# Kernel optimization log

Measured on AMD Instinct MI355X. Metric: run time of the kernel, lower is better.

Reference implementation:

```python
import jax, jax.numpy as jnp
import numpy as np

N, F_IN, HID, NH1, NCLS = 8192, 256, 64, 4, 16
LRELU_ALPHA = 0.2  # tf.nn.leaky_relu default


def setup_inputs() -> dict:
    key = jax.random.key(0)
    ks = jax.random.split(key, 12)
    s = 0.05
    seq = jax.random.normal(ks[0], (1, N, F_IN), jnp.float32)
    # sparse-ish adjacency -> additive mask bias (0 on edges, -1e9 elsewhere)
    adj = jax.random.uniform(ks[1], (N, N)) < 0.005
    adj = adj | jnp.eye(N, dtype=bool)
    bias_mat = jnp.where(adj, 0.0, -1e9).astype(jnp.float32)[None]  # [1,N,N]
    return {
        "seq": seq,
        "bias_mat": bias_mat,
        "W1": jax.random.normal(ks[2], (NH1, F_IN, HID), jnp.float32) * s,
        "a1_src": jax.random.normal(ks[3], (NH1, HID, 1), jnp.float32) * s,
        "a1_dst": jax.random.normal(ks[4], (NH1, HID, 1), jnp.float32) * s,
        "b1_src": jnp.zeros((NH1, 1), jnp.float32),
        "b1_dst": jnp.zeros((NH1, 1), jnp.float32),
        "bias1": jnp.zeros((NH1, HID), jnp.float32),
        "W2": jax.random.normal(ks[5], (1, NH1 * HID, NCLS), jnp.float32) * s,
        "a2_src": jax.random.normal(ks[6], (1, NCLS, 1), jnp.float32) * s,
        "a2_dst": jax.random.normal(ks[7], (1, NCLS, 1), jnp.float32) * s,
        "b2_src": jnp.zeros((1, 1), jnp.float32),
        "b2_dst": jnp.zeros((1, 1), jnp.float32),
        "bias2": jnp.zeros((1, NCLS), jnp.float32),
    }


def _gat_layer(x, bias_mat, W, a_src, a_dst, b_src, b_dst, bias_out):
    # x: [N, Fin]; W: [nh, Fin, H]; bias_mat: [1, N, N]
    fts = jnp.einsum('nf,hfd->hnd', x, W)                      # Conv1D(k=1, no bias)
    f1 = jnp.einsum('hnd,hdo->hno', fts, a_src) + b_src[:, None, :]  # [nh,N,1]
    f2 = jnp.einsum('hnd,hdo->hno', fts, a_dst) + b_dst[:, None, :]  # [nh,N,1]
    logits = f1 + jnp.swapaxes(f2, 1, 2)                       # [nh,N,N]
    coefs = jax.nn.softmax(jax.nn.leaky_relu(logits, LRELU_ALPHA) + bias_mat, axis=-1)
    vals = jnp.einsum('hnm,hmd->hnd', coefs, fts)              # [nh,N,H]
    return vals + bias_out[:, None, :]


def reference(seq, bias_mat, W1, a1_src, a1_dst, b1_src, b1_dst, bias1,
              W2, a2_src, a2_dst, b2_src, b2_dst, bias2):
    x = seq[0]  # [N, F_IN]; batch dim is 1
    # layer 1: NH1 heads, elu activation, concat over heads
    h = jax.nn.elu(_gat_layer(x, bias_mat, W1, a1_src, a1_dst, b1_src, b1_dst, bias1))
    h1 = jnp.transpose(h, (1, 0, 2)).reshape(N, NH1 * HID)     # tf.concat(heads, -1)
    # output layer: 1 head, identity activation, averaged over final heads (=1)
    out = _gat_layer(h1, bias_mat, W2, a2_src, a2_dst, b2_src, b2_dst, bias2)
    logits = out[0] / 1.0                                      # add_n/final_sum
    return logits[None]  # [1, N, NCLS]
```

## Files before the change

kernel.cpp:

```cpp
#include <hip/hip_runtime.h>
#include <hip/hip_bf16.h>
#include <math.h>

#define NN    8192
#define FIN   256
#define HID   64
#define NH    4
#define NC    16
#define MAXD  128
#define ALPHA 0.2f
#define KC    32

typedef float nfloat4 __attribute__((ext_vector_type(4)));
__device__ __forceinline__ float4 ldnt4(const float4* p) {
    nfloat4 v = __builtin_nontemporal_load((const nfloat4*)p);
    return make_float4(v.x, v.y, v.z, v.w);
}

__global__ __launch_bounds__(256) void k_gemm(
    const float* __restrict__ seq, const float* __restrict__ W1,
    const float* __restrict__ a1s, const float* __restrict__ a1d,
    const float* __restrict__ b1s, const float* __restrict__ b1d,
    float* __restrict__ fts1, float* __restrict__ f1v, float* __restrict__ f2v)
{
    __shared__ union {
        struct { float xsT[KC][68]; float w[KC][68]; } g;
        struct { float r1[64][17];  float r2[64][17]; } gr;
    } S;
    const int t = threadIdx.x, b = blockIdx.x;
    const int head = b & 3, rowbase = (b >> 2) * 64;
    const int tr = t >> 4, tc = t & 15;

    float acc[4][4] = {};
    for (int kc = 0; kc < FIN / KC; ++kc) {
        #pragma unroll
        for (int i = 0; i < 2; ++i) {
            const int lin = t + i*256;
            const int row = lin >> 3, kq = lin & 7;
            const float4 v = *(const float4*)(seq + (size_t)(rowbase + row)*FIN + kc*KC + kq*4);
            S.g.xsT[kq*4+0][row] = v.x;
            S.g.xsT[kq*4+1][row] = v.y;
            S.g.xsT[kq*4+2][row] = v.z;
            S.g.xsT[kq*4+3][row] = v.w;
        }
        #pragma unroll
        for (int i = 0; i < 2; ++i) {
            const int lin = t + i*256;
            const int k = lin >> 4, dq = lin & 15;
            *(float4*)&S.g.w[k][dq*4] =
                *(const float4*)(W1 + ((size_t)head*FIN + kc*KC + k)*HID + dq*4);
        }
        __syncthreads();
        #pragma unroll 8
        for (int k = 0; k < KC; ++k) {
            const float4 aa = *(const float4*)&S.g.xsT[k][tr*4];
            const float4 bb = *(const float4*)&S.g.w[k][tc*4];
            acc[0][0] += aa.x*bb.x; acc[0][1] += aa.x*bb.y; acc[0][2] += aa.x*bb.z; acc[0][3] += aa.x*bb.w;
            acc[1][0] += aa.y*bb.x; acc[1][1] += aa.y*bb.y; acc[1][2] += aa.y*bb.z; acc[1][3] += aa.y*bb.w;
            acc[2][0] += aa.z*bb.x; acc[2][1] += aa.z*bb.y; acc[2][2] += aa.z*bb.z; acc[2][3] += aa.z*bb.w;
            acc[3][0] += aa.w*bb.x; acc[3][1] += aa.w*bb.y; acc[3][2] += aa.w*bb.z; acc[3][3] += aa.w*bb.w;
        }
        __syncthreads();
    }
    float p1[4], p2[4];
    #pragma unroll
    for (int i = 0; i < 4; ++i) {
        const int node = rowbase + tr*4 + i;
        float4 o; o.x = acc[i][0]; o.y = acc[i][1]; o.z = acc[i][2]; o.w = acc[i][3];
        *(float4*)&fts1[((size_t)node*NH + head)*HID + tc*4] = o;
        float s1 = 0.f, s2 = 0.f;
        #pragma unroll
        for (int j = 0; j < 4; ++j) {
            s1 += acc[i][j] * a1s[head*HID + tc*4 + j];
            s2 += acc[i][j] * a1d[head*HID + tc*4 + j];
        }
        p1[i] = s1; p2[i] = s2;
    }
    #pragma unroll
    for (int i = 0; i < 4; ++i) {
        S.gr.r1[tr*4 + i][tc] = p1[i];
        S.gr.r2[tr*4 + i][tc] = p2[i];
    }
    __syncthreads();
    if (t < 64) {
        float s1 = b1s[head], s2 = b1d[head];
        #pragma unroll
        for (int q = 0; q < 16; ++q) { s1 += S.gr.r1[t][q]; s2 += S.gr.r2[t][q]; }
        f1v[(rowbase + t)*NH + head] = s1;
        f2v[(rowbase + t)*NH + head] = s2;
    }
}

__global__ __launch_bounds__(256) void k_scan_attn(
    const float* __restrict__ bias, const float* __restrict__ fts1,
    const float* __restrict__ f1v4, const float* __restrict__ f2v4,
    const float* __restrict__ bias1, const float* __restrict__ W2,
    const float* __restrict__ a2s, const float* __restrict__ a2d,
    const float* __restrict__ b2s, const float* __restrict__ b2d,
    int* __restrict__ deg, int* __restrict__ cols,
    float* __restrict__ fts2, float* __restrict__ g1, float* __restrict__ g2)
{
    __shared__ int    colsS[4][MAXD];
    __shared__ float4 coefS[4][MAXD];
    __shared__ float  h1S[4][NH*HID];

    const int t = threadIdx.x, w = t >> 6, lane = t & 63;
    const int row = blockIdx.x*4 + w;
    const unsigned long long lt = (1ull << lane) - 1ull;

    colsS[w][lane] = 0; colsS[w][64 + lane] = 0;

    const float4* rp = (const float4*)(bias + (size_t)row * NN);
    float4 vv[8];
    #pragma unroll
    for (int k = 0; k < 8; ++k) vv[k] = ldnt4(rp + k*64 + lane);
    int base = 0;
    #pragma unroll
    for (int s = 0; s < 4; ++s) {
        #pragma unroll
        for (int k = 0; k < 8; ++k) {
            const float4 v = vv[k];
            if (s < 3) vv[k] = ldnt4(rp + ((s+1)*8 + k)*64 + lane);
            const unsigned long long m0 = __ballot(v.x == 0.f);
            const unsigned long long m1 = __ballot(v.y == 0.f);
            const unsigned long long m2 = __ballot(v.z == 0.f);
            const unsigned long long m3 = __ballot(v.w == 0.f);
            const int cb = ((s*8 + k)*64 + lane)*4;
            int p = base + __popcll(m0&lt) + __popcll(m1&lt)
                         + __popcll(m2&lt) + __popcll(m3&lt);
            if (v.x == 0.f) { if (p < MAXD) colsS[w][p] = cb;     ++p; }
            if (v.y == 0.f) { if (p < MAXD) colsS[w][p] = cb + 1; ++p; }
            if (v.z == 0.f) { if (p < MAXD) colsS[w][p] = cb + 2; ++p; }
            if (v.w == 0.f) { if (p < MAXD) colsS[w][p] = cb + 3; ++p; }
            base += __popcll(m0) + __popcll(m1) + __popcll(m2) + __popcll(m3);
        }
    }
    const int d = base < MAXD ? base : MAXD;
    if (lane == 0) deg[row] = d;
    cols[(size_t)row*MAXD + lane]      = colsS[w][lane];
    cols[(size_t)row*MAXD + 64 + lane] = colsS[w][64 + lane];

    const float4 f1 = *(const float4*)(f1v4 + (size_t)row*NH);
    const int c0 = colsS[w][lane], c1 = colsS[w][64 + lane];
    float4 s0 = make_float4(-1e30f,-1e30f,-1e30f,-1e30f), s1 = s0;
    if (lane < d) {
        const float4 F = *(const float4*)(f2v4 + (size_t)c0*NH);
        float x;
        x = f1.x + F.x; s0.x = x > 0.f ? x : ALPHA*x;
        x = f1.y + F.y; s0.y = x > 0.f ? x : ALPHA*x;
        x = f1.z + F.z; s0.z = x > 0.f ? x : ALPHA*x;
        x = f1.w + F.w; s0.w = x > 0.f ? x : ALPHA*x;
    }
    if (lane + 64 < d) {
        const float4 F = *(const float4*)(f2v4 + (size_t)c1*NH);
        float x;
        x = f1.x + F.x; s1.x = x > 0.f ? x : ALPHA*x;
        x = f1.y + F.y; s1.y = x > 0.f ? x : ALPHA*x;
        x = f1.z + F.z; s1.z = x > 0.f ? x : ALPHA*x;
        x = f1.w + F.w; s1.w = x > 0.f ? x : ALPHA*x;
    }
    float4 m;
    m.x = fmaxf(s0.x, s1.x); m.y = fmaxf(s0.y, s1.y);
    m.z = fmaxf(s0.z, s1.z); m.w = fmaxf(s0.w, s1.w);
    #pragma unroll
    for (int off = 32; off; off >>= 1) {
        m.x = fmaxf(m.x, __shfl_xor(m.x, off));
        m.y = fmaxf(m.y, __shfl_xor(m.y, off));
        m.z = fmaxf(m.z, __shfl_xor(m.z, off));
        m.w = fmaxf(m.w, __shfl_xor(m.w, off));
    }
    float4 p0 = make_float4(0,0,0,0), p1 = p0;
    if (lane < d) {
        p0.x = expf(s0.x - m.x); p0.y = expf(s0.y - m.y);
        p0.z = expf(s0.z - m.z); p0.w = expf(s0.w - m.w);
    }
    if (lane + 64 < d) {
        p1.x = expf(s1.x - m.x); p1.y = expf(s1.y - m.y);
        p1.z = expf(s1.z - m.z); p1.w = expf(s1.w - m.w);
    }
    coefS[w][lane]      = p0;
    coefS[w][64 + lane] = p1;
    float4 sum;
    sum.x = p0.x + p1.x; sum.y = p0.y + p1.y;
    sum.z = p0.z + p1.z; sum.w = p0.w + p1.w;
    #pragma unroll
    for (int off = 32; off; off >>= 1) {
        sum.x += __shfl_xor(sum.x, off);
        sum.y += __shfl_xor(sum.y, off);
        sum.z += __shfl_xor(sum.z, off);
        sum.w += __shfl_xor(sum.w, off);
    }
    const float4 inv = make_float4(1.f/sum.x, 1.f/sum.y, 1.f/sum.z, 1.f/sum.w);

    float a0 = 0.f, a1 = 0.f, a2 = 0.f, a3 = 0.f;
    #pragma unroll 4
    for (int e = 0; e < d; ++e) {
        const float4 cf = coefS[w][e];
        const float* fp = fts1 + (size_t)colsS[w][e]*(NH*HID);
        a0 += cf.x * fp[0*HID + lane];
        a1 += cf.y * fp[1*HID + lane];
        a2 += cf.z * fp[2*HID + lane];
        a3 += cf.w * fp[3*HID + lane];
    }
    float v;
    v = a0*inv.x + bias1[0*HID + lane]; h1S[w][0*HID + lane] = v > 0.f ? v : expm1f(v);
    v = a1*inv.y + bias1[1*HID + lane]; h1S[w][1*HID + lane] = v > 0.f ? v : expm1f(v);
    v = a2*inv.z + bias1[2*HID + lane]; h1S[w][2*HID + lane] = v > 0.f ? v : expm1f(v);
    v = a3*inv.w + bias1[3*HID + lane]; h1S[w][3*HID + lane] = v > 0.f ? v : expm1f(v);

    const int part = lane >> 4, c = lane & 15;
    float s = 0.f;
    #pragma unroll 8
    for (int q = 0; q < 64; ++q)
        s += h1S[w][part*64 + q] * W2[(part*64 + q)*NC + c];
    s += __shfl_xor(s, 16);
    s += __shfl_xor(s, 32);
    if (lane < NC) fts2[(size_t)row*NC + lane] = s;

    float t1 = (lane < NC) ? s * a2s[lane] : 0.f;
    float t2 = (lane < NC) ? s * a2d[lane] : 0.f;
    #pragma unroll
    for (int off = 8; off; off >>= 1) {
        t1 += __shfl_xor(t1, off);
        t2 += __shfl_xor(t2, off);
    }
    if (lane == 0) { g1[row] = t1 + b2s[0]; g2[row] = t2 + b2d[0]; }
}

__global__ __launch_bounds__(256) void k_attn2(
    const float* __restrict__ fts2, const float* __restrict__ g1,
    const float* __restrict__ g2, const float* __restrict__ bias2,
    const int* __restrict__ deg, const int* __restrict__ cols,
    float* __restrict__ out)
{
    __shared__ int   colsS[4][MAXD];
    __shared__ float coefS[4][MAXD];
    const int t = threadIdx.x, w = t >> 6, lane = t & 63;
    const int i = blockIdx.x*4 + w;
    const int d = deg[i];
    for (int e = lane; e < MAXD; e += 64) colsS[w][e] = (e < d) ? cols[(size_t)i*MAXD + e] : 0;

    const float g1i = g1[i];
    float sc0 = -1e30f, sc1 = -1e30f;
    if (lane < d)      { const float x = g1i + g2[colsS[w][lane]];    sc0 = x > 0.f ? x : ALPHA*x; }
    if (lane + 64 < d) { const float x = g1i + g2[colsS[w][lane+64]]; sc1 = x > 0.f ? x : ALPHA*x; }
    float m = fmaxf(sc0, sc1);
    #pragma unroll
    for (int off = 32; off; off >>= 1) m = fmaxf(m, __shfl_xor(m, off));
    const float p0 = (lane      < d) ? expf(sc0 - m) : 0.f;
    const float p1 = (lane + 64 < d) ? expf(sc1 - m) : 0.f;
    coefS[w][lane] = p0; coefS[w][lane + 64] = p1;
    float sum = p0 + p1;
    #pragma unroll
    for (int off = 32; off; off >>= 1) sum += __shfl_xor(sum, off);
    const float inv = 1.f / sum;

    const int eg = lane >> 4, c = lane & 15;
    float acc = 0.f;
    #pragma unroll 2
    for (int e0 = 0; e0 < d; e0 += 4) {
        const int e = e0 + eg;
        if (e < d) acc += coefS[w][e] * fts2[(size_t)colsS[w][e]*NC + c];
    }
    acc += __shfl_xor(acc, 16);
    acc += __shfl_xor(acc, 32);
    if (lane < NC) out[(size_t)i*NC + lane] = acc*inv + bias2[lane];
}

extern "C" void kernel_launch(void* const* d_in, const int* in_sizes, int n_in,
                              void* d_out, int out_size, void* d_ws, size_t ws_size,
                              hipStream_t stream)
{
    const float* seq   = (const float*)d_in[0];
    const float* bias  = (const float*)d_in[1];
    const float* W1    = (const float*)d_in[2];
    const float* a1s   = (const float*)d_in[3];
    const float* a1d   = (const float*)d_in[4];
    const float* b1s   = (const float*)d_in[5];
    const float* b1d   = (const float*)d_in[6];
    const float* bias1 = (const float*)d_in[7];
    const float* W2    = (const float*)d_in[8];
    const float* a2s   = (const float*)d_in[9];
    const float* a2d   = (const float*)d_in[10];
    const float* b2s   = (const float*)d_in[11];
    const float* b2d   = (const float*)d_in[12];
    const float* bias2 = (const float*)d_in[13];

    char* ws = (char*)d_ws;
    int*   deg  = (int*)ws;    ws += (size_t)NN * 4;
    int*   cols = (int*)ws;    ws += (size_t)NN * MAXD * 4;
    float* fts1 = (float*)ws;  ws += (size_t)NN * NH * HID * 4;
    float* f1v  = (float*)ws;  ws += (size_t)NN * NH * 4;
    float* f2v  = (float*)ws;  ws += (size_t)NN * NH * 4;
    float* fts2 = (float*)ws;  ws += (size_t)NN * NC * 4;
    float* g1   = (float*)ws;  ws += (size_t)NN * 4;
    float* g2   = (float*)ws;  ws += (size_t)NN * 4;

    hipLaunchKernelGGL(k_gemm, dim3(512), dim3(256), 0, stream,
                       seq, W1, a1s, a1d, b1s, b1d, fts1, f1v, f2v);
    hipLaunchKernelGGL(k_scan_attn, dim3(NN/4), dim3(256), 0, stream,
                       bias, fts1, f1v, f2v, bias1, W2, a2s, a2d, b2s, b2d,
                       deg, cols, fts2, g1, g2);
    hipLaunchKernelGGL(k_attn2, dim3(NN/4), dim3(256), 0, stream,
                       fts2, g1, g2, bias2, deg, cols, (float*)d_out);
}
```

Baseline: 113.9 us.

## Pipeline adjacency scan with GEMM and attention in chunked launches, store features as bf16

Splits the adjacency-scan pass into row chunks and interleaves each chunk with other work in the same launch. The first chunk is scanned alongside the layer-1 GEMM, and every later chunk alongside the attention for the previous chunk. This is meant to overlap the bandwidth-heavy bias-matrix scan with compute-heavy stages. It also stores the layer-1 features as bf16 to halve gather traffic, and reworks the gather so each lane handles one head with packed loads. The cost is more kernel launches and reduced feature precision in the aggregation.

Measured after the change: 136.4 us. 19.8% more time.

```diff
diff --git a/kernel.cpp b/kernel.cpp
--- a/kernel.cpp
+++ b/kernel.cpp
@@ -10,106 +10,27 @@
 #define MAXD  128
 #define ALPHA 0.2f
 #define KC    32
+#define CH    2048
+#define CBLK  (CH/4)
 
 typedef float nfloat4 __attribute__((ext_vector_type(4)));
 __device__ __forceinline__ float4 ldnt4(const float4* p) {
     nfloat4 v = __builtin_nontemporal_load((const nfloat4*)p);
     return make_float4(v.x, v.y, v.z, v.w);
 }
-
-__global__ __launch_bounds__(256) void k_gemm(
-    const float* __restrict__ seq, const float* __restrict__ W1,
-    const float* __restrict__ a1s, const float* __restrict__ a1d,
-    const float* __restrict__ b1s, const float* __restrict__ b1d,
-    float* __restrict__ fts1, float* __restrict__ f1v, float* __restrict__ f2v)
-{
-    __shared__ union {
-        struct { float xsT[KC][68]; float w[KC][68]; } g;
-        struct { float r1[64][17];  float r2[64][17]; } gr;
-    } S;
-    const int t = threadIdx.x, b = blockIdx.x;
-    const int head = b & 3, rowbase = (b >> 2) * 64;
-    const int tr = t >> 4, tc = t & 15;
-
-    float acc[4][4] = {};
-    for (int kc = 0; kc < FIN / KC; ++kc) {
-        #pragma unroll
-        for (int i = 0; i < 2; ++i) {
-            const int lin = t + i*256;
-            const int row = lin >> 3, kq = lin & 7;
-            const float4 v = *(const float4*)(seq + (size_t)(rowbase + row)*FIN + kc*KC + kq*4);
-            S.g.xsT[kq*4+0][row] = v.x;
-            S.g.xsT[kq*4+1][row] = v.y;
-            S.g.xsT[kq*4+2][row] = v.z;
-            S.g.xsT[kq*4+3][row] = v.w;
-        }
-        #pragma unroll
-        for (int i = 0; i < 2; ++i) {
-            const int lin = t + i*256;
-            const int k = lin >> 4, dq = lin & 15;
-            *(float4*)&S.g.w[k][dq*4] =
-                *(const float4*)(W1 + ((size_t)head*FIN + kc*KC + k)*HID + dq*4);
-        }
-        __syncthreads();
-        #pragma unroll 8
-        for (int k = 0; k < KC; ++k) {
-            const float4 aa = *(const float4*)&S.g.xsT[k][tr*4];
-            const float4 bb = *(const float4*)&S.g.w[k][tc*4];
-            acc[0][0] += aa.x*bb.x; acc[0][1] += aa.x*bb.y; acc[0][2] += aa.x*bb.z; acc[0][3] += aa.x*bb.w;
-            acc[1][0] += aa.y*bb.x; acc[1][1] += aa.y*bb.y; acc[1][2] += aa.y*bb.z; acc[1][3] += aa.y*bb.w;
-            acc[2][0] += aa.z*bb.x; acc[2][1] += aa.z*bb.y; acc[2][2] += aa.z*bb.z; acc[2][3] += aa.z*bb.w;
-            acc[3][0] += aa.w*bb.x; acc[3][1] += aa.w*bb.y; acc[3][2] += aa.w*bb.z; acc[3][3] += aa.w*bb.w;
-        }
-        __syncthreads();
-    }
-    float p1[4], p2[4];
-    #pragma unroll
-    for (int i = 0; i < 4; ++i) {
-        const int node = rowbase + tr*4 + i;
-        float4 o; o.x = acc[i][0]; o.y = acc[i][1]; o.z = acc[i][2]; o.w = acc[i][3];
-        *(float4*)&fts1[((size_t)node*NH + head)*HID + tc*4] = o;
-        float s1 = 0.f, s2 = 0.f;
-        #pragma unroll
-        for (int j = 0; j < 4; ++j) {
-            s1 += acc[i][j] * a1s[head*HID + tc*4 + j];
-            s2 += acc[i][j] * a1d[head*HID + tc*4 + j];
-        }
-        p1[i] = s1; p2[i] = s2;
-    }
-    #pragma unroll
-    for (int i = 0; i < 4; ++i) {
-        S.gr.r1[tr*4 + i][tc] = p1[i];
-        S.gr.r2[tr*4 + i][tc] = p2[i];
-    }
-    __syncthreads();
-    if (t < 64) {
-        float s1 = b1s[head], s2 = b1d[head];
-        #pragma unroll
-        for (int q = 0; q < 16; ++q) { s1 += S.gr.r1[t][q]; s2 += S.gr.r2[t][q]; }
-        f1v[(rowbase + t)*NH + head] = s1;
-        f2v[(rowbase + t)*NH + head] = s2;
-    }
-}
-
-__global__ __launch_bounds__(256) void k_scan_attn(
-    const float* __restrict__ bias, const float* __restrict__ fts1,
-    const float* __restrict__ f1v4, const float* __restrict__ f2v4,
-    const float* __restrict__ bias1, const float* __restrict__ W2,
-    const float* __restrict__ a2s, const float* __restrict__ a2d,
-    const float* __restrict__ b2s, const float* __restrict__ b2d,
-    int* __restrict__ deg, int* __restrict__ cols,
-    float* __restrict__ fts2, float* __restrict__ g1, float* __restrict__ g2)
-{
-    __shared__ int    colsS[4][MAXD];
-    __shared__ float4 coefS[4][MAXD];
-    __shared__ float  h1S[4][NH*HID];
-
-    const int t = threadIdx.x, w = t >> 6, lane = t & 63;
-    const int row = blockIdx.x*4 + w;
+__device__ __forceinline__ ushort f2bf(float x) {
+    __hip_bfloat16 h = __float2bfloat16(x);
+    return *reinterpret_cast<ushort*>(&h);
+}
+__device__ __forceinline__ float bfhi(unsigned u) { return __uint_as_float(u & 0xffff0000u); }
+__device__ __forceinline__ float bflo(unsigned u) { return __uint_as_float(u << 16); }
+
+__device__ __forceinline__ void scan_row(
+    int row, int lane, int* colsW,
+    const float* __restrict__ bias, int* __restrict__ deg, int* __restrict__ cols)
+{
     const unsigned long long lt = (1ull << lane) - 1ull;
-
-    colsS[w][lane] = 0; colsS[w][64 + lane] = 0;
-
+    colsW[lane] = 0; colsW[64 + lane] = 0;
     const float4* rp = (const float4*)(bias + (size_t)row * NN);
     float4 vv[8];
     #pragma unroll
@@ -128,20 +49,35 @@
             const int cb = ((s*8 + k)*64 + lane)*4;
             int p = base + __popcll(m0&lt) + __popcll(m1&lt)
                          + __popcll(m2&lt) + __popcll(m3&lt);
-            if (v.x == 0.f) { if (p < MAXD) colsS[w][p] = cb;     ++p; }
-            if (v.y == 0.f) { if (p < MAXD) colsS[w][p] = cb + 1; ++p; }
-            if (v.z == 0.f) { if (p < MAXD) colsS[w][p] = cb + 2; ++p; }
-            if (v.w == 0.f) { if (p < MAXD) colsS[w][p] = cb + 3; ++p; }
+            if (v.x == 0.f) { if (p < MAXD) colsW[p] = cb;     ++p; }
+            if (v.y == 0.f) { if (p < MAXD) colsW[p] = cb + 1; ++p; }
+            if (v.z == 0.f) { if (p < MAXD) colsW[p] = cb + 2; ++p; }
+            if (v.w == 0.f) { if (p < MAXD) colsW[p] = cb + 3; ++p; }
             base += __popcll(m0) + __popcll(m1) + __popcll(m2) + __popcll(m3);
         }
     }
     const int d = base < MAXD ? base : MAXD;
     if (lane == 0) deg[row] = d;
-    cols[(size_t)row*MAXD + lane]      = colsS[w][lane];
-    cols[(size_t)row*MAXD + 64 + lane] = colsS[w][64 + lane];
+    cols[(size_t)row*MAXD + lane]      = colsW[lane];
+    cols[(size_t)row*MAXD + 64 + lane] = colsW[64 + lane];
+}
+
+__device__ __forceinline__ void attn_row(
+    int row, int lane, int* colsW, float4* coefW, float* h1W ,
+    const ushort* __restrict__ fts1g, const float* __restrict__ f1v4,
+    const float* __restrict__ f2v4, const float* __restrict__ bias1,
+    const float* __restrict__ W2, const float* __restrict__ a2s,
+    const float* __restrict__ a2d, const float* __restrict__ b2s,
+    const float* __restrict__ b2d, const int* __restrict__ deg,
+    const int* __restrict__ cols, float* __restrict__ fts2,
+    float* __restrict__ g1, float* __restrict__ g2)
+{
+    const int d = deg[row];
+    const int c0 = cols[(size_t)row*MAXD + lane];
+    const int c1 = cols[(size_t)row*MAXD + 64 + lane];
+    colsW[lane] = c0; colsW[64 + lane] = c1;
 
     const float4 f1 = *(const float4*)(f1v4 + (size_t)row*NH);
-    const int c0 = colsS[w][lane], c1 = colsS[w][64 + lane];
     float4 s0 = make_float4(-1e30f,-1e30f,-1e30f,-1e30f), s1 = s0;
     if (lane < d) {
         const float4 F = *(const float4*)(f2v4 + (size_t)c0*NH);
@@ -178,8 +114,7 @@
         p1.x = expf(s1.x - m.x); p1.y = expf(s1.y - m.y);
         p1.z = expf(s1.z - m.z); p1.w = expf(s1.w - m.w);
     }
-    coefS[w][lane]      = p0;
-    coefS[w][64 + lane] = p1;
+    coefW[lane] = p0; coefW[64 + lane] = p1;
     float4 sum;
     sum.x = p0.x + p1.x; sum.y = p0.y + p1.y;
     sum.z = p0.z + p1.z; sum.w = p0.w + p1.w;
@@ -190,29 +125,33 @@
         sum.z += __shfl_xor(sum.z, off);
         sum.w += __shfl_xor(sum.w, off);
     }
-    const float4 inv = make_float4(1.f/sum.x, 1.f/sum.y, 1.f/sum.z, 1.f/sum.w);
+    const int h = lane >> 4;
+    const float invh = (h==0) ? 1.f/sum.x : (h==1) ? 1.f/sum.y
+                     : (h==2) ? 1.f/sum.z : 1.f/sum.w;
 
     float a0 = 0.f, a1 = 0.f, a2 = 0.f, a3 = 0.f;
-    #pragma unroll 4
+    #pragma unroll 8
     for (int e = 0; e < d; ++e) {
-        const float4 cf = coefS[w][e];
-        const float* fp = fts1 + (size_t)colsS[w][e]*(NH*HID);
-        a0 += cf.x * fp[0*HID + lane];
-        a1 += cf.y * fp[1*HID + lane];
-        a2 += cf.z * fp[2*HID + lane];
-        a3 += cf.w * fp[3*HID + lane];
-    }
+        const float4 q4 = coefW[e];
+        const float cf = (h==0) ? q4.x : (h==1) ? q4.y : (h==2) ? q4.z : q4.w;
+        const uint2 q = *(const uint2*)(fts1g + (size_t)colsW[e]*(NH*HID) + lane*4);
+        a0 += cf * bflo(q.x); a1 += cf * bfhi(q.x);
+        a2 += cf * bflo(q.y); a3 += cf * bfhi(q.y);
+    }
+    const float4 bv = *(const float4*)(bias1 + lane*4);
+    float4 ev;
     float v;
-    v = a0*inv.x + bias1[0*HID + lane]; h1S[w][0*HID + lane] = v > 0.f ? v : expm1f(v);
-    v = a1*inv.y + bias1[1*HID + lane]; h1S[w][1*HID + lane] = v > 0.f ? v : expm1f(v);
-    v = a2*inv.z + bias1[2*HID + lane]; h1S[w][2*HID + lane] = v > 0.f ? v : expm1f(v);
-    v = a3*inv.w + bias1[3*HID + lane]; h1S[w][3*HID + lane] = v > 0.f ? v : expm1f(v);
+    v = a0*invh + bv.x; ev.x = v > 0.f ? v : expm1f(v);
+    v = a1*invh + bv.y; ev.y = v > 0.f ? v : expm1f(v);
+    v = a2*invh + bv.z; ev.z = v > 0.f ? v : expm1f(v);
+    v = a3*invh + bv.w; ev.w = v > 0.f ? v : expm1f(v);
+    *(float4*)&h1W[h*68 + (lane & 15)*4] = ev;
 
     const int part = lane >> 4, c = lane & 15;
     float s = 0.f;
     #pragma unroll 8
     for (int q = 0; q < 64; ++q)
-        s += h1S[w][part*64 + q] * W2[(part*64 + q)*NC + c];
+        s += h1W[part*68 + q] * W2[(part*64 + q)*NC + c];
     s += __shfl_xor(s, 16);
     s += __shfl_xor(s, 32);
     if (lane < NC) fts2[(size_t)row*NC + lane] = s;
@@ -225,6 +164,123 @@
         t2 += __shfl_xor(t2, off);
     }
     if (lane == 0) { g1[row] = t1 + b2s[0]; g2[row] = t2 + b2d[0]; }
+}
+
+struct AttnLDS {
+    int    colsS[4][MAXD];
+    float4 coefS[4][MAXD];
+    float  h1S[4][NH*68];
+};
+
+__global__ __launch_bounds__(256, 4) void k_gemm_scan(
+    const float* __restrict__ seq, const float* __restrict__ W1,
+    const float* __restrict__ a1s, const float* __restrict__ a1d,
+    const float* __restrict__ b1s, const float* __restrict__ b1d,
+    const float* __restrict__ bias,
+    ushort* __restrict__ fts1g, float* __restrict__ f1v, float* __restrict__ f2v,
+    int* __restrict__ deg, int* __restrict__ cols)
+{
+    __shared__ union {
+        struct { float xsT[KC][68]; float w[KC][68]; } g;
+        struct { float r1[64][17];  float r2[64][17]; } gr;
+        int colsS[4][MAXD];
+    } S;
+    const int t = threadIdx.x, bid = blockIdx.x;
+    const int w = t >> 6, lane = t & 63;
+
+    if (bid & 1) {
+        scan_row((bid >> 1)*4 + w, lane, &S.colsS[w][0], bias, deg, cols);
+        return;
+    }
+    const int b = bid >> 1;
+    const int head = b & 3, rowbase = (b >> 2) * 64;
+    const int tr = t >> 4, tc = t & 15;
+
+    float acc[4][4] = {};
+    for (int kc = 0; kc < FIN / KC; ++kc) {
+        #pragma unroll
+        for (int i = 0; i < 2; ++i) {
+            const int lin = t + i*256;
+            const int row = lin >> 3, kq = lin & 7;
+            const float4 v = *(const float4*)(seq + (size_t)(rowbase + row)*FIN + kc*KC + kq*4);
+            S.g.xsT[kq*4+0][row] = v.x;
+            S.g.xsT[kq*4+1][row] = v.y;
+            S.g.xsT[kq*4+2][row] = v.z;
+            S.g.xsT[kq*4+3][row] = v.w;
+        }
+        #pragma unroll
+        for (int i = 0; i < 2; ++i) {
+            const int lin = t + i*256;
+            const int k = lin >> 4, dq = lin & 15;
+            *(float4*)&S.g.w[k][dq*4] =
+                *(const float4*)(W1 + ((size_t)head*FIN + kc*KC + k)*HID + dq*4);
+        }
+        __syncthreads();
+        #pragma unroll 8
+        for (int k = 0; k < KC; ++k) {
+            const float4 aa = *(const float4*)&S.g.xsT[k][tr*4];
+            const float4 bb = *(const float4*)&S.g.w[k][tc*4];
+            acc[0][0] += aa.x*bb.x; acc[0][1] += aa.x*bb.y; acc[0][2] += aa.x*bb.z; acc[0][3] += aa.x*bb.w;
+            acc[1][0] += aa.y*bb.x; acc[1][1] += aa.y*bb.y; acc[1][2] += aa.y*bb.z; acc[1][3] += aa.y*bb.w;
+            acc[2][0] += aa.z*bb.x; acc[2][1] += aa.z*bb.y; acc[2][2] += aa.z*bb.z; acc[2][3] += aa.z*bb.w;
+            acc[3][0] += aa.w*bb.x; acc[3][1] += aa.w*bb.y; acc[3][2] += aa.w*bb.z; acc[3][3] += aa.w*bb.w;
+        }
+        __syncthreads();
+    }
+    float p1[4], p2[4];
+    #pragma unroll
+    for (int i = 0; i < 4; ++i) {
+        const int node = rowbase + tr*4 + i;
+        ushort4 o;
+        o.x = f2bf(acc[i][0]); o.y = f2bf(acc[i][1]);
+        o.z = f2bf(acc[i][2]); o.w = f2bf(acc[i][3]);
+        *(ushort4*)&fts1g[(size_t)node*(NH*HID) + head*HID + tc*4] = o;
+        float s1 = 0.f, s2 = 0.f;
+        #pragma unroll
+        for (int j = 0; j < 4; ++j) {
+            s1 += acc[i][j] * a1s[head*HID + tc*4 + j];
+            s2 += acc[i][j] * a1d[head*HID + tc*4 + j];
+        }
+        p1[i] = s1; p2[i] = s2;
+    }
+    #pragma unroll
+    for (int i = 0; i < 4; ++i) {
+        S.gr.r1[tr*4 + i][tc] = p1[i];
+        S.gr.r2[tr*4 + i][tc] = p2[i];
+    }
+    __syncthreads();
+    if (t < 64) {
+        float s1 = b1s[head], s2 = b1d[head];
+        #pragma unroll
+        for (int q = 0; q < 16; ++q) { s1 += S.gr.r1[t][q]; s2 += S.gr.r2[t][q]; }
+        f1v[(rowbase + t)*NH + head] = s1;
+        f2v[(rowbase + t)*NH + head] = s2;
+    }
+}
+
+__global__ __launch_bounds__(256, 4) void k_stage(
+    const float* __restrict__ bias, const ushort* __restrict__ fts1g,
+    const float* __restrict__ f1v4, const float* __restrict__ f2v4,
+    const float* __restrict__ bias1, const float* __restrict__ W2,
+    const float* __restrict__ a2s, const float* __restrict__ a2d,
+    const float* __restrict__ b2s, const float* __restrict__ b2d,
+    int* __restrict__ deg, int* __restrict__ cols,
+    float* __restrict__ fts2, float* __restrict__ g1, float* __restrict__ g2,
+    int scanBase, int attnBase, int nScanBlk)
+{
+    __shared__ AttnLDS S;
+    const int t = threadIdx.x, bid = blockIdx.x;
+    const int w = t >> 6, lane = t & 63;
+
+    if (nScanBlk && !(bid & 1)) {
+        scan_row(scanBase + (bid >> 1)*4 + w, lane, &S.colsS[w][0], bias, deg, cols);
+        return;
+    }
+    const int aidx = nScanBlk ? (bid >> 1) : bid;
+    attn_row(attnBase + aidx*4 + w, lane,
+             &S.colsS[w][0], &S.coefS[w][0], &S.h1S[w][0],
+             fts1g, f1v4, f2v4, bias1, W2, a2s, a2d, b2s, b2d,
+             deg, cols, fts2, g1, g2);
 }
 
 __global__ __launch_bounds__(256) void k_attn2(
@@ -287,20 +343,28 @@
     const float* bias2 = (const float*)d_in[13];
 
     char* ws = (char*)d_ws;
-    int*   deg  = (int*)ws;    ws += (size_t)NN * 4;
-    int*   cols = (int*)ws;    ws += (size_t)NN * MAXD * 4;
-    float* fts1 = (float*)ws;  ws += (size_t)NN * NH * HID * 4;
-    float* f1v  = (float*)ws;  ws += (size_t)NN * NH * 4;
-    float* f2v  = (float*)ws;  ws += (size_t)NN * NH * 4;
-    float* fts2 = (float*)ws;  ws += (size_t)NN * NC * 4;
-    float* g1   = (float*)ws;  ws += (size_t)NN * 4;
-    float* g2   = (float*)ws;  ws += (size_t)NN * 4;
-
-    hipLaunchKernelGGL(k_gemm, dim3(512), dim3(256), 0, stream,
-                       seq, W1, a1s, a1d, b1s, b1d, fts1, f1v, f2v);
-    hipLaunchKernelGGL(k_scan_attn, dim3(NN/4), dim3(256), 0, stream,
-                       bias, fts1, f1v, f2v, bias1, W2, a2s, a2d, b2s, b2d,
-                       deg, cols, fts2, g1, g2);
+    int*    deg   = (int*)ws;    ws += (size_t)NN * 4;
+    int*    cols  = (int*)ws;    ws += (size_t)NN * MAXD * 4;
+    ushort* fts1g = (ushort*)ws; ws += (size_t)NN * NH * HID * 2;
+    float*  f1v   = (float*)ws;  ws += (size_t)NN * NH * 4;
+    float*  f2v   = (float*)ws;  ws += (size_t)NN * NH * 4;
+    float*  fts2  = (float*)ws;  ws += (size_t)NN * NC * 4;
+    float*  g1    = (float*)ws;  ws += (size_t)NN * 4;
+    float*  g2    = (float*)ws;  ws += (size_t)NN * 4;
+
+    hipLaunchKernelGGL(k_gemm_scan, dim3(1024), dim3(256), 0, stream,
+                       seq, W1, a1s, a1d, b1s, b1d, bias,
+                       fts1g, f1v, f2v, deg, cols);
+    for (int c = 1; c < 4; ++c) {
+        hipLaunchKernelGGL(k_stage, dim3(2*CBLK), dim3(256), 0, stream,
+                           bias, fts1g, f1v, f2v, bias1, W2, a2s, a2d, b2s, b2d,
+                           deg, cols, fts2, g1, g2,
+                           c*CH, (c-1)*CH, CBLK);
+    }
+    hipLaunchKernelGGL(k_stage, dim3(CBLK), dim3(256), 0, stream,
+                       bias, fts1g, f1v, f2v, bias1, W2, a2s, a2d, b2s, b2d,
+                       deg, cols, fts2, g1, g2,
+                       0, 3*CH, 0);
     hipLaunchKernelGGL(k_attn2, dim3(NN/4), dim3(256), 0, stream,
                        fts2, g1, g2, bias2, deg, cols, (float*)d_out);
 }
```
